# Kernel optimization log

Measured on AMD Instinct MI355X. Metric: run time of the kernel, lower is better.

## Reference

```python
import jax, jax.numpy as jnp
import numpy as np

N = 1_000_000
M = 8
HX = HY = 64
U = V = 512
L = 96 // 6  # latent_size // 6 = 16


def setup_inputs() -> dict:
    key = jax.random.key(0)
    ks = jax.random.split(key, 11)
    r = jax.random.uniform(ks[0], (N,), dtype=jnp.float32)
    m = jax.random.randint(ks[1], (N,), 0, M, dtype=jnp.int32)
    h = jax.random.uniform(ks[2], (N, 2), dtype=jnp.float32, minval=-1.0, maxval=1.0)
    u = jax.random.uniform(ks[3], (N,), dtype=jnp.float32)
    v = jax.random.uniform(ks[4], (N,), dtype=jnp.float32)
    Fxy = jax.random.normal(ks[5], (M, HX, HY, L), dtype=jnp.float32)
    Fxu = jax.random.normal(ks[6], (M, HX, U, L), dtype=jnp.float32)
    Fxv = jax.random.normal(ks[7], (M, HX, V, L), dtype=jnp.float32)
    Fyu = jax.random.normal(ks[8], (M, HY, U, L), dtype=jnp.float32)
    Fyv = jax.random.normal(ks[9], (M, HY, V, L), dtype=jnp.float32)
    Fuv = jax.random.normal(ks[10], (M, U, V, L), dtype=jnp.float32)
    return {"r": r, "m": m, "h": h, "u": u, "v": v,
            "Fxy": Fxy, "Fxu": Fxu, "Fxv": Fxv,
            "Fyu": Fyu, "Fyv": Fyv, "Fuv": Fuv}


def _bilinear(x, m, i, j, I, J):
    # x: [M, I, J, L]; m,i,j: [N]; wrap-around bilinear interpolation
    i1 = jnp.floor(i).astype(jnp.int32)
    j1 = jnp.floor(j).astype(jnp.int32)
    i2 = (i1 + 1) % I
    j2 = (j1 + 1) % J
    ir = (i - i1)[..., None]  # [N,1]
    jr = (j - j1)[..., None]
    top = x[m, i1, j1, :] * (1 - ir) + x[m, i2, j1, :] * ir
    bot = x[m, i1, j2, :] * (1 - ir) + x[m, i2, j2, :] * ir
    return top * (1 - jr) + bot * jr


def reference(r, m, h, u, v, Fxy, Fxu, Fxv, Fyu, Fyv, Fuv) -> jnp.ndarray:
    ind_hx = (h[..., 0] + 1) / 2 * HX
    ind_hy = (h[..., 1] + 1) / 2 * HY
    ind_hx = jnp.where(ind_hx == HX, HX - 1, ind_hx)
    ind_hy = jnp.where(ind_hy == HY, HY - 1, ind_hy)
    ind_u = u * U
    ind_v = v * V
    ind_u = jnp.where(ind_u == U, U - 1, ind_u)
    ind_v = jnp.where(ind_v == V, V - 1, ind_v)
    latent = jnp.concatenate([
        _bilinear(Fxy, m, ind_hx, ind_hy, HX, HY),
        _bilinear(Fxu, m, ind_hx, ind_u, HX, U),
        _bilinear(Fxv, m, ind_hx, ind_v, HX, V),
        _bilinear(Fyu, m, ind_hy, ind_u, HY, U),
        _bilinear(Fyv, m, ind_hy, ind_v, HY, V),
        _bilinear(Fuv, m, ind_u, ind_v, U, V),
    ], axis=-1)  # [N, 6*L]
    return latent
```

## Files before the change

kernel.cpp:

```cpp
#include <hip/hip_runtime.h>

#define HXc 64
#define HYc 64
#define Uc  512
#define Vc  512
#define Lc  16
#define NBUCK 8192

typedef float v4f __attribute__((ext_vector_type(4)));


__device__ __forceinline__ void compute_inds(float h0, float h1, float uu, float vv,
                                             float& ix, float& iy, float& iu, float& iv) {
    ix = (h0 + 1.0f) * 0.5f * (float)HXc; if (ix == (float)HXc) ix = (float)(HXc - 1);
    iy = (h1 + 1.0f) * 0.5f * (float)HYc; if (iy == (float)HYc) iy = (float)(HYc - 1);
    iu = uu * (float)Uc;                  if (iu == (float)Uc)  iu = (float)(Uc - 1);
    iv = vv * (float)Vc;                  if (iv == (float)Vc)  iv = (float)(Vc - 1);
}

__device__ __forceinline__ int bucket_of(int mm, float iu, float iv) {
    int us = ((int)iu) >> 4;
    int vs = ((int)iv) >> 4;
    return (((mm << 5) | vs) << 5) | us;
}


__global__ __launch_bounds__(256) void zero_kernel(int* __restrict__ counts) {
    int i = blockIdx.x * 256 + threadIdx.x;
    if (i < NBUCK) counts[i] = 0;
}


__global__ __launch_bounds__(256) void hist_kernel(
    const int* __restrict__ m_arr, const float* __restrict__ u_arr,
    const float* __restrict__ v_arr, int* __restrict__ counts, int N)
{
    int n = blockIdx.x * 256 + threadIdx.x;
    if (n >= N) return;
    float iu = u_arr[n] * (float)Uc; if (iu == (float)Uc) iu = (float)(Uc - 1);
    float iv = v_arr[n] * (float)Vc; if (iv == (float)Vc) iv = (float)(Vc - 1);
    atomicAdd(&counts[bucket_of(m_arr[n], iu, iv)], 1);
}


__global__ __launch_bounds__(1024) void scan_kernel(
    const int* __restrict__ counts, int* __restrict__ cursors)
{
    __shared__ int lds[1024];
    int t = threadIdx.x;
    int base = t * 8;
    int s = 0;
    #pragma unroll
    for (int k = 0; k < 8; ++k) s += counts[base + k];
    lds[t] = s;
    __syncthreads();
    for (int off = 1; off < 1024; off <<= 1) {
        int val = (t >= off) ? lds[t - off] : 0;
        __syncthreads();
        lds[t] += val;
        __syncthreads();
    }
    int run = lds[t] - s;
    #pragma unroll
    for (int k = 0; k < 8; ++k) {
        cursors[base + k] = run;
        run += counts[base + k];
    }
}


__global__ __launch_bounds__(256) void scatter_kernel(
    const int* __restrict__ m_arr, const float* __restrict__ h,
    const float* __restrict__ u_arr, const float* __restrict__ v_arr,
    int* __restrict__ cursors,
    v4f* __restrict__ inds4, int* __restrict__ m_s, int* __restrict__ outidx,
    int N)
{
    int n = blockIdx.x * 256 + threadIdx.x;
    if (n >= N) return;
    float h0 = h[2 * n], h1 = h[2 * n + 1];
    float ix, iy, iu, iv;
    compute_inds(h0, h1, u_arr[n], v_arr[n], ix, iy, iu, iv);
    int mm = m_arr[n];
    int b  = bucket_of(mm, iu, iv);
    int pos = atomicAdd(&cursors[b], 1);
    v4f rec; rec.x = ix; rec.y = iy; rec.z = iu; rec.w = iv;
    inds4[pos]  = rec;
    m_s[pos]    = mm;
    outidx[pos] = n;
}


struct BL {
    const float* a11; const float* a21; const float* a12; const float* a22;
    float ir, jr;
};

__device__ __forceinline__ v4f ld4(const float* p) {
    return *reinterpret_cast<const v4f*>(p);
}

__device__ __forceinline__ BL mk(const float* __restrict__ base, int mm,
                                 float fi, float fj, int I, int J, int chan) {
    BL b;
    int i1 = (int)floorf(fi);
    int j1 = (int)floorf(fj);
    b.ir = fi - (float)i1;
    b.jr = fj - (float)j1;
    int i2 = (i1 + 1 == I) ? 0 : (i1 + 1);
    int j2 = (j1 + 1 == J) ? 0 : (j1 + 1);
    const float* p = base + ((size_t)mm * I * J) * Lc + chan;
    b.a11 = p + (size_t)(i1 * J + j1) * Lc;
    b.a21 = p + (size_t)(i2 * J + j1) * Lc;
    b.a12 = p + (size_t)(i1 * J + j2) * Lc;
    b.a22 = p + (size_t)(i2 * J + j2) * Lc;
    return b;
}

__device__ __forceinline__ v4f blend(v4f c11, v4f c21, v4f c12, v4f c22,
                                     float ir, float jr) {
    float oir = 1.0f - ir;
    float ojr = 1.0f - jr;
    v4f top = c11 * oir + c21 * ir;
    v4f bot = c12 * oir + c22 * ir;
    return top * ojr + bot * jr;
}

__global__ __launch_bounds__(256) void main_kernel(
    const v4f* __restrict__ inds4, const int* __restrict__ m_s,
    const int* __restrict__ outidx,
    const float* __restrict__ Fxy, const float* __restrict__ Fxu,
    const float* __restrict__ Fxv, const float* __restrict__ Fyu,
    const float* __restrict__ Fyv, const float* __restrict__ Fuv,
    float* __restrict__ out, int N, int nwg)
{
    int bid = blockIdx.x;
    int q = nwg >> 3, r = nwg & 7;
    int xcd = bid & 7, idx = bid >> 3;
    int swz = (xcd < r) ? (xcd * (q + 1) + idx) : (r * (q + 1) + (xcd - r) * q + idx);

    int t   = swz * 256 + threadIdx.x;
    int k   = t >> 2;
    int sub = t & 3;
    if (k >= N) return;

    v4f inds = inds4[k];
    int mm   = m_s[k];
    int n    = outidx[k];
    float ind_hx = inds.x, ind_hy = inds.y, ind_u = inds.z, ind_v = inds.w;

    int chan = sub * 4;

    BL b0 = mk(Fxy, mm, ind_hx, ind_hy, HXc, HYc, chan);
    BL b1 = mk(Fxu, mm, ind_hx, ind_u,  HXc, Uc,  chan);
    BL b2 = mk(Fxv, mm, ind_hx, ind_v,  HXc, Vc,  chan);
    BL b3 = mk(Fyu, mm, ind_hy, ind_u,  HYc, Uc,  chan);
    BL b4 = mk(Fyv, mm, ind_hy, ind_v,  HYc, Vc,  chan);
    BL b5 = mk(Fuv, mm, ind_u,  ind_v,  Uc,  Vc,  chan);

    v4f c0a = ld4(b0.a11); v4f c0b = ld4(b0.a21); v4f c0c = ld4(b0.a12); v4f c0d = ld4(b0.a22);
    v4f c1a = ld4(b1.a11); v4f c1b = ld4(b1.a21); v4f c1c = ld4(b1.a12); v4f c1d = ld4(b1.a22);
    v4f c2a = ld4(b2.a11); v4f c2b = ld4(b2.a21); v4f c2c = ld4(b2.a12); v4f c2d = ld4(b2.a22);
    v4f c3a = ld4(b3.a11); v4f c3b = ld4(b3.a21); v4f c3c = ld4(b3.a12); v4f c3d = ld4(b3.a22);
    v4f c4a = ld4(b4.a11); v4f c4b = ld4(b4.a21); v4f c4c = ld4(b4.a12); v4f c4d = ld4(b4.a22);
    v4f c5a = ld4(b5.a11); v4f c5b = ld4(b5.a21); v4f c5c = ld4(b5.a12); v4f c5d = ld4(b5.a22);

    __builtin_amdgcn_sched_barrier(0);

    float* o = out + (size_t)n * 96 + chan;

    *reinterpret_cast<v4f*>(o + 0 * Lc) = blend(c0a, c0b, c0c, c0d, b0.ir, b0.jr);
    *reinterpret_cast<v4f*>(o + 1 * Lc) = blend(c1a, c1b, c1c, c1d, b1.ir, b1.jr);
    *reinterpret_cast<v4f*>(o + 2 * Lc) = blend(c2a, c2b, c2c, c2d, b2.ir, b2.jr);
    *reinterpret_cast<v4f*>(o + 3 * Lc) = blend(c3a, c3b, c3c, c3d, b3.ir, b3.jr);
    *reinterpret_cast<v4f*>(o + 4 * Lc) = blend(c4a, c4b, c4c, c4d, b4.ir, b4.jr);
    *reinterpret_cast<v4f*>(o + 5 * Lc) = blend(c5a, c5b, c5c, c5d, b5.ir, b5.jr);
}


__global__ __launch_bounds__(256) void flat_kernel(
    const int*   __restrict__ m_arr,
    const float* __restrict__ h,
    const float* __restrict__ u_arr,
    const float* __restrict__ v_arr,
    const float* __restrict__ Fxy, const float* __restrict__ Fxu,
    const float* __restrict__ Fxv, const float* __restrict__ Fyu,
    const float* __restrict__ Fyv, const float* __restrict__ Fuv,
    float* __restrict__ out, int N)
{
    int tid = blockIdx.x * blockDim.x + threadIdx.x;
    int n   = tid >> 2;
    int sub = tid & 3;
    if (n >= N) return;

    float h0 = h[2 * n], h1 = h[2 * n + 1];
    float ind_hx, ind_hy, ind_u, ind_v;
    compute_inds(h0, h1, u_arr[n], v_arr[n], ind_hx, ind_hy, ind_u, ind_v);
    int mm = m_arr[n];
    int chan = sub * 4;

    BL b0 = mk(Fxy, mm, ind_hx, ind_hy, HXc, HYc, chan);
    BL b1 = mk(Fxu, mm, ind_hx, ind_u,  HXc, Uc,  chan);
    BL b2 = mk(Fxv, mm, ind_hx, ind_v,  HXc, Vc,  chan);
    BL b3 = mk(Fyu, mm, ind_hy, ind_u,  HYc, Uc,  chan);
    BL b4 = mk(Fyv, mm, ind_hy, ind_v,  HYc, Vc,  chan);
    BL b5 = mk(Fuv, mm, ind_u,  ind_v,  Uc,  Vc,  chan);

    v4f c0a = ld4(b0.a11); v4f c0b = ld4(b0.a21); v4f c0c = ld4(b0.a12); v4f c0d = ld4(b0.a22);
    v4f c1a = ld4(b1.a11); v4f c1b = ld4(b1.a21); v4f c1c = ld4(b1.a12); v4f c1d = ld4(b1.a22);
    v4f c2a = ld4(b2.a11); v4f c2b = ld4(b2.a21); v4f c2c = ld4(b2.a12); v4f c2d = ld4(b2.a22);
    v4f c3a = ld4(b3.a11); v4f c3b = ld4(b3.a21); v4f c3c = ld4(b3.a12); v4f c3d = ld4(b3.a22);
    v4f c4a = ld4(b4.a11); v4f c4b = ld4(b4.a21); v4f c4c = ld4(b4.a12); v4f c4d = ld4(b4.a22);
    v4f c5a = ld4(b5.a11); v4f c5b = ld4(b5.a21); v4f c5c = ld4(b5.a12); v4f c5d = ld4(b5.a22);

    __builtin_amdgcn_sched_barrier(0);

    float* o = out + (size_t)n * 96 + chan;
    *reinterpret_cast<v4f*>(o + 0 * Lc) = blend(c0a, c0b, c0c, c0d, b0.ir, b0.jr);
    *reinterpret_cast<v4f*>(o + 1 * Lc) = blend(c1a, c1b, c1c, c1d, b1.ir, b1.jr);
    *reinterpret_cast<v4f*>(o + 2 * Lc) = blend(c2a, c2b, c2c, c2d, b2.ir, b2.jr);
    *reinterpret_cast<v4f*>(o + 3 * Lc) = blend(c3a, c3b, c3c, c3d, b3.ir, b3.jr);
    *reinterpret_cast<v4f*>(o + 4 * Lc) = blend(c4a, c4b, c4c, c4d, b4.ir, b4.jr);
    *reinterpret_cast<v4f*>(o + 5 * Lc) = blend(c5a, c5b, c5c, c5d, b5.ir, b5.jr);
}


extern "C" void kernel_launch(void* const* d_in, const int* in_sizes, int n_in,
                              void* d_out, int out_size, void* d_ws, size_t ws_size,
                              hipStream_t stream) {
    const int*   m_arr = (const int*)  d_in[1];
    const float* h     = (const float*)d_in[2];
    const float* u_arr = (const float*)d_in[3];
    const float* v_arr = (const float*)d_in[4];
    const float* Fxy   = (const float*)d_in[5];
    const float* Fxu   = (const float*)d_in[6];
    const float* Fxv   = (const float*)d_in[7];
    const float* Fyu   = (const float*)d_in[8];
    const float* Fyv   = (const float*)d_in[9];
    const float* Fuv   = (const float*)d_in[10];
    float* out = (float*)d_out;

    int N = in_sizes[0];

    size_t off_counts  = 0;
    size_t off_cursors = off_counts  + (size_t)NBUCK * 4;
    size_t off_inds4   = off_cursors + (size_t)NBUCK * 4;
    size_t off_ms      = off_inds4   + (size_t)N * 16;
    size_t off_outidx  = off_ms      + (size_t)N * 4;
    size_t needed      = off_outidx  + (size_t)N * 4;

    if (d_ws == nullptr || ws_size < needed) {
        int total_threads = 4 * N;
        dim3 block(256);
        dim3 grid((total_threads + 255) / 256);
        flat_kernel<<<grid, block, 0, stream>>>(m_arr, h, u_arr, v_arr,
                                                Fxy, Fxu, Fxv, Fyu, Fyv, Fuv, out, N);
        return;
    }

    char* ws = (char*)d_ws;
    int* counts  = (int*)(ws + off_counts);
    int* cursors = (int*)(ws + off_cursors);
    v4f* inds4   = (v4f*)(ws + off_inds4);
    int* m_s     = (int*)(ws + off_ms);
    int* outidx  = (int*)(ws + off_outidx);

    dim3 blk(256);
    dim3 grdN((N + 255) / 256);

    zero_kernel<<<dim3((NBUCK + 255) / 256), blk, 0, stream>>>(counts);
    hist_kernel<<<grdN, blk, 0, stream>>>(m_arr, u_arr, v_arr, counts, N);
    scan_kernel<<<dim3(1), dim3(1024), 0, stream>>>(counts, cursors);
    scatter_kernel<<<grdN, blk, 0, stream>>>(m_arr, h, u_arr, v_arr, cursors,
                                             inds4, m_s, outidx, N);

    int total_threads = 4 * N;
    int nwg = (total_threads + 255) / 256;
    main_kernel<<<dim3(nwg), blk, 0, stream>>>(inds4, m_s, outidx,
                                               Fxy, Fxu, Fxv, Fyu, Fyv, Fuv,
                                               out, N, nwg);
}
```

Baseline: 787.2 us.

## Convert feature grids to fp16 each call and gather half-precision texels

Each call now converts all six fp32 feature grids to fp16 in the workspace. The main gather kernel then reads 8-element half vectors, with two threads per point instead of four, and blends in fp32. The scatter packs the material id and output index into one 32-bit key, and the histogram kernel handles four points per thread with vector loads. The aim is to halve gather bandwidth and per-point index traffic, at the cost of converting roughly 150 MB of grids (about 38M floats) on every call and of fp16 rounding error.

Result: no change. 779.9 us (-0.9%).

```diff
diff --git a/kernel.cpp b/kernel.cpp
--- a/kernel.cpp
+++ b/kernel.cpp
@@ -7,7 +7,8 @@
 #define Lc  16
 #define NBUCK 8192
 
-typedef float v4f __attribute__((ext_vector_type(4)));
+typedef float    v4f __attribute__((ext_vector_type(4)));
+typedef _Float16 h8  __attribute__((ext_vector_type(8)));
 
 
 __device__ __forceinline__ void compute_inds(float h0, float h1, float uu, float vv,
@@ -25,6 +26,21 @@
 }
 
 
+__global__ __launch_bounds__(256) void convert_kernel(
+    const float* __restrict__ src, _Float16* __restrict__ dst, int n8)
+{
+    int i = blockIdx.x * 256 + threadIdx.x;
+    if (i >= n8) return;
+    const v4f* s4 = reinterpret_cast<const v4f*>(src);
+    v4f a = s4[2 * i];
+    v4f b = s4[2 * i + 1];
+    h8 o;
+    o[0] = (_Float16)a.x; o[1] = (_Float16)a.y; o[2] = (_Float16)a.z; o[3] = (_Float16)a.w;
+    o[4] = (_Float16)b.x; o[5] = (_Float16)b.y; o[6] = (_Float16)b.z; o[7] = (_Float16)b.w;
+    *reinterpret_cast<h8*>(dst + 8 * (size_t)i) = o;
+}
+
+
 __global__ __launch_bounds__(256) void zero_kernel(int* __restrict__ counts) {
     int i = blockIdx.x * 256 + threadIdx.x;
     if (i < NBUCK) counts[i] = 0;
@@ -35,11 +51,25 @@
     const int* __restrict__ m_arr, const float* __restrict__ u_arr,
     const float* __restrict__ v_arr, int* __restrict__ counts, int N)
 {
-    int n = blockIdx.x * 256 + threadIdx.x;
-    if (n >= N) return;
-    float iu = u_arr[n] * (float)Uc; if (iu == (float)Uc) iu = (float)(Uc - 1);
-    float iv = v_arr[n] * (float)Vc; if (iv == (float)Vc) iv = (float)(Vc - 1);
-    atomicAdd(&counts[bucket_of(m_arr[n], iu, iv)], 1);
+    int base = (blockIdx.x * 256 + threadIdx.x) * 4;
+    if (base >= N) return;
+    if (base + 3 < N) {
+        v4f u4 = *reinterpret_cast<const v4f*>(u_arr + base);
+        v4f vv4 = *reinterpret_cast<const v4f*>(v_arr + base);
+        int4 m4 = *reinterpret_cast<const int4*>(m_arr + base);
+        #pragma unroll
+        for (int k = 0; k < 4; ++k) {
+            float iu = ((const float*)&u4)[k] * (float)Uc; if (iu == (float)Uc) iu = (float)(Uc - 1);
+            float iv = ((const float*)&vv4)[k] * (float)Vc; if (iv == (float)Vc) iv = (float)(Vc - 1);
+            atomicAdd(&counts[bucket_of(((const int*)&m4)[k], iu, iv)], 1);
+        }
+    } else {
+        for (int n = base; n < N; ++n) {
+            float iu = u_arr[n] * (float)Uc; if (iu == (float)Uc) iu = (float)(Uc - 1);
+            float iv = v_arr[n] * (float)Vc; if (iv == (float)Vc) iv = (float)(Vc - 1);
+            atomicAdd(&counts[bucket_of(m_arr[n], iu, iv)], 1);
+        }
+    }
 }
 
 
@@ -73,7 +103,7 @@
     const int* __restrict__ m_arr, const float* __restrict__ h,
     const float* __restrict__ u_arr, const float* __restrict__ v_arr,
     int* __restrict__ cursors,
-    v4f* __restrict__ inds4, int* __restrict__ m_s, int* __restrict__ outidx,
+    v4f* __restrict__ inds4, unsigned int* __restrict__ keys,
     int N)
 {
     int n = blockIdx.x * 256 + threadIdx.x;
@@ -85,9 +115,116 @@
     int b  = bucket_of(mm, iu, iv);
     int pos = atomicAdd(&cursors[b], 1);
     v4f rec; rec.x = ix; rec.y = iy; rec.z = iu; rec.w = iv;
-    inds4[pos]  = rec;
-    m_s[pos]    = mm;
-    outidx[pos] = n;
+    inds4[pos] = rec;
+    keys[pos]  = (unsigned int)n | ((unsigned int)mm << 24);
+}
+
+
+struct F8 { v4f lo, hi; };
+
+__device__ __forceinline__ F8 cvt8(h8 x) {
+    F8 r;
+    r.lo.x = (float)x[0]; r.lo.y = (float)x[1]; r.lo.z = (float)x[2]; r.lo.w = (float)x[3];
+    r.hi.x = (float)x[4]; r.hi.y = (float)x[5]; r.hi.z = (float)x[6]; r.hi.w = (float)x[7];
+    return r;
+}
+
+struct BLH {
+    const _Float16* a11; const _Float16* a21; const _Float16* a12; const _Float16* a22;
+    float ir, jr;
+};
+
+__device__ __forceinline__ BLH mkh(const _Float16* __restrict__ base, int mm,
+                                   float fi, float fj, int I, int J, int chan) {
+    BLH b;
+    int i1 = (int)floorf(fi);
+    int j1 = (int)floorf(fj);
+    b.ir = fi - (float)i1;
+    b.jr = fj - (float)j1;
+    int i2 = (i1 + 1 == I) ? 0 : (i1 + 1);
+    int j2 = (j1 + 1 == J) ? 0 : (j1 + 1);
+    const _Float16* p = base + ((size_t)mm * I * J) * Lc + chan;
+    b.a11 = p + (size_t)(i1 * J + j1) * Lc;
+    b.a21 = p + (size_t)(i2 * J + j1) * Lc;
+    b.a12 = p + (size_t)(i1 * J + j2) * Lc;
+    b.a22 = p + (size_t)(i2 * J + j2) * Lc;
+    return b;
+}
+
+__device__ __forceinline__ h8 ldh(const _Float16* p) {
+    return *reinterpret_cast<const h8*>(p);
+}
+
+__device__ __forceinline__ F8 blend8(h8 h11, h8 h21, h8 h12, h8 h22, float ir, float jr) {
+    F8 c11 = cvt8(h11), c21 = cvt8(h21), c12 = cvt8(h12), c22 = cvt8(h22);
+    float oir = 1.0f - ir, ojr = 1.0f - jr;
+    F8 r;
+    r.lo = (c11.lo * oir + c21.lo * ir) * ojr + (c12.lo * oir + c22.lo * ir) * jr;
+    r.hi = (c11.hi * oir + c21.hi * ir) * ojr + (c12.hi * oir + c22.hi * ir) * jr;
+    return r;
+}
+
+__global__ __launch_bounds__(256) void main_f16_kernel(
+    const v4f* __restrict__ inds4, const unsigned int* __restrict__ keys,
+    const _Float16* __restrict__ Hxy, const _Float16* __restrict__ Hxu,
+    const _Float16* __restrict__ Hxv, const _Float16* __restrict__ Hyu,
+    const _Float16* __restrict__ Hyv, const _Float16* __restrict__ Huv,
+    float* __restrict__ out, int N, int nwg)
+{
+    int bid = blockIdx.x;
+    int q = nwg >> 3, r = nwg & 7;
+    int xcd = bid & 7, idx = bid >> 3;
+    int swz = (xcd < r) ? (xcd * (q + 1) + idx) : (r * (q + 1) + (xcd - r) * q + idx);
+
+    int t   = swz * 256 + threadIdx.x;
+    int k   = t >> 1;
+    int sub = t & 1;
+    if (k >= N) return;
+
+    v4f inds = inds4[k];
+    unsigned int key = keys[k];
+    int mm = (int)(key >> 24);
+    int n  = (int)(key & 0xFFFFFFu);
+    float ind_hx = inds.x, ind_hy = inds.y, ind_u = inds.z, ind_v = inds.w;
+
+    int chan = sub * 8;
+
+    BLH b0 = mkh(Hxy, mm, ind_hx, ind_hy, HXc, HYc, chan);
+    BLH b1 = mkh(Hxu, mm, ind_hx, ind_u,  HXc, Uc,  chan);
+    BLH b2 = mkh(Hxv, mm, ind_hx, ind_v,  HXc, Vc,  chan);
+    BLH b3 = mkh(Hyu, mm, ind_hy, ind_u,  HYc, Uc,  chan);
+    BLH b4 = mkh(Hyv, mm, ind_hy, ind_v,  HYc, Vc,  chan);
+    BLH b5 = mkh(Huv, mm, ind_u,  ind_v,  Uc,  Vc,  chan);
+
+    h8 c0a = ldh(b0.a11); h8 c0b = ldh(b0.a21); h8 c0c = ldh(b0.a12); h8 c0d = ldh(b0.a22);
+    h8 c1a = ldh(b1.a11); h8 c1b = ldh(b1.a21); h8 c1c = ldh(b1.a12); h8 c1d = ldh(b1.a22);
+    h8 c2a = ldh(b2.a11); h8 c2b = ldh(b2.a21); h8 c2c = ldh(b2.a12); h8 c2d = ldh(b2.a22);
+    h8 c3a = ldh(b3.a11); h8 c3b = ldh(b3.a21); h8 c3c = ldh(b3.a12); h8 c3d = ldh(b3.a22);
+    h8 c4a = ldh(b4.a11); h8 c4b = ldh(b4.a21); h8 c4c = ldh(b4.a12); h8 c4d = ldh(b4.a22);
+    h8 c5a = ldh(b5.a11); h8 c5b = ldh(b5.a21); h8 c5c = ldh(b5.a12); h8 c5d = ldh(b5.a22);
+
+    __builtin_amdgcn_sched_barrier(0);
+
+    float* o = out + (size_t)n * 96 + chan;
+
+    F8 r0 = blend8(c0a, c0b, c0c, c0d, b0.ir, b0.jr);
+    *reinterpret_cast<v4f*>(o + 0 * Lc)     = r0.lo;
+    *reinterpret_cast<v4f*>(o + 0 * Lc + 4) = r0.hi;
+    F8 r1 = blend8(c1a, c1b, c1c, c1d, b1.ir, b1.jr);
+    *reinterpret_cast<v4f*>(o + 1 * Lc)     = r1.lo;
+    *reinterpret_cast<v4f*>(o + 1 * Lc + 4) = r1.hi;
+    F8 r2 = blend8(c2a, c2b, c2c, c2d, b2.ir, b2.jr);
+    *reinterpret_cast<v4f*>(o + 2 * Lc)     = r2.lo;
+    *reinterpret_cast<v4f*>(o + 2 * Lc + 4) = r2.hi;
+    F8 r3 = blend8(c3a, c3b, c3c, c3d, b3.ir, b3.jr);
+    *reinterpret_cast<v4f*>(o + 3 * Lc)     = r3.lo;
+    *reinterpret_cast<v4f*>(o + 3 * Lc + 4) = r3.hi;
+    F8 r4 = blend8(c4a, c4b, c4c, c4d, b4.ir, b4.jr);
+    *reinterpret_cast<v4f*>(o + 4 * Lc)     = r4.lo;
+    *reinterpret_cast<v4f*>(o + 4 * Lc + 4) = r4.hi;
+    F8 r5 = blend8(c5a, c5b, c5c, c5d, b5.ir, b5.jr);
+    *reinterpret_cast<v4f*>(o + 5 * Lc)     = r5.lo;
+    *reinterpret_cast<v4f*>(o + 5 * Lc + 4) = r5.hi;
 }
 
 
@@ -126,9 +263,8 @@
     return top * ojr + bot * jr;
 }
 
-__global__ __launch_bounds__(256) void main_kernel(
-    const v4f* __restrict__ inds4, const int* __restrict__ m_s,
-    const int* __restrict__ outidx,
+__global__ __launch_bounds__(256) void main_f32_kernel(
+    const v4f* __restrict__ inds4, const unsigned int* __restrict__ keys,
     const float* __restrict__ Fxy, const float* __restrict__ Fxu,
     const float* __restrict__ Fxv, const float* __restrict__ Fyu,
     const float* __restrict__ Fyv, const float* __restrict__ Fuv,
@@ -145,8 +281,9 @@
     if (k >= N) return;
 
     v4f inds = inds4[k];
-    int mm   = m_s[k];
-    int n    = outidx[k];
+    unsigned int key = keys[k];
+    int mm = (int)(key >> 24);
+    int n  = (int)(key & 0xFFFFFFu);
     float ind_hx = inds.x, ind_hy = inds.y, ind_u = inds.z, ind_v = inds.w;
 
     int chan = sub * 4;
@@ -168,7 +305,6 @@
     __builtin_amdgcn_sched_barrier(0);
 
     float* o = out + (size_t)n * 96 + chan;
-
     *reinterpret_cast<v4f*>(o + 0 * Lc) = blend(c0a, c0b, c0c, c0d, b0.ir, b0.jr);
     *reinterpret_cast<v4f*>(o + 1 * Lc) = blend(c1a, c1b, c1c, c1d, b1.ir, b1.jr);
     *reinterpret_cast<v4f*>(o + 2 * Lc) = blend(c2a, c2b, c2c, c2d, b2.ir, b2.jr);
@@ -242,41 +378,87 @@
 
     int N = in_sizes[0];
 
-    size_t off_counts  = 0;
+    const size_t SZ_xy = (size_t)8 * 64 * 64 * 16;
+    const size_t SZ_mid = (size_t)8 * 64 * 512 * 16;
+    const size_t SZ_uv = (size_t)8 * 512 * 512 * 16;
+    const size_t SZ_half_total = SZ_xy + 4 * SZ_mid + SZ_uv;
+
+    size_t off_hxy   = 0;
+    size_t off_hxu   = off_hxy + SZ_xy * 2;
+    size_t off_hxv   = off_hxu + SZ_mid * 2;
+    size_t off_hyu   = off_hxv + SZ_mid * 2;
+    size_t off_hyv   = off_hyu + SZ_mid * 2;
+    size_t off_huv   = off_hyv + SZ_mid * 2;
+    size_t off_counts  = off_huv + SZ_uv * 2;
     size_t off_cursors = off_counts  + (size_t)NBUCK * 4;
     size_t off_inds4   = off_cursors + (size_t)NBUCK * 4;
-    size_t off_ms      = off_inds4   + (size_t)N * 16;
-    size_t off_outidx  = off_ms      + (size_t)N * 4;
-    size_t needed      = off_outidx  + (size_t)N * 4;
-
-    if (d_ws == nullptr || ws_size < needed) {
-        int total_threads = 4 * N;
-        dim3 block(256);
-        dim3 grid((total_threads + 255) / 256);
-        flat_kernel<<<grid, block, 0, stream>>>(m_arr, h, u_arr, v_arr,
-                                                Fxy, Fxu, Fxv, Fyu, Fyv, Fuv, out, N);
-        return;
-    }
-
-    char* ws = (char*)d_ws;
-    int* counts  = (int*)(ws + off_counts);
-    int* cursors = (int*)(ws + off_cursors);
-    v4f* inds4   = (v4f*)(ws + off_inds4);
-    int* m_s     = (int*)(ws + off_ms);
-    int* outidx  = (int*)(ws + off_outidx);
+    size_t off_keys    = off_inds4   + (size_t)N * 16;
+    size_t need_f16    = off_keys    + (size_t)N * 4;
+
+    size_t f32_counts  = 0;
+    size_t f32_cursors = f32_counts  + (size_t)NBUCK * 4;
+    size_t f32_inds4   = f32_cursors + (size_t)NBUCK * 4;
+    size_t f32_keys    = f32_inds4   + (size_t)N * 16;
+    size_t need_f32    = f32_keys    + (size_t)N * 4;
 
     dim3 blk(256);
     dim3 grdN((N + 255) / 256);
-
-    zero_kernel<<<dim3((NBUCK + 255) / 256), blk, 0, stream>>>(counts);
-    hist_kernel<<<grdN, blk, 0, stream>>>(m_arr, u_arr, v_arr, counts, N);
-    scan_kernel<<<dim3(1), dim3(1024), 0, stream>>>(counts, cursors);
-    scatter_kernel<<<grdN, blk, 0, stream>>>(m_arr, h, u_arr, v_arr, cursors,
-                                             inds4, m_s, outidx, N);
-
-    int total_threads = 4 * N;
-    int nwg = (total_threads + 255) / 256;
-    main_kernel<<<dim3(nwg), blk, 0, stream>>>(inds4, m_s, outidx,
-                                               Fxy, Fxu, Fxv, Fyu, Fyv, Fuv,
-                                               out, N, nwg);
-}
+    char* ws = (char*)d_ws;
+
+    if (ws != nullptr && ws_size >= need_f16) {
+        _Float16* Hxy = (_Float16*)(ws + off_hxy);
+        _Float16* Hxu = (_Float16*)(ws + off_hxu);
+        _Float16* Hxv = (_Float16*)(ws + off_hxv);
+        _Float16* Hyu = (_Float16*)(ws + off_hyu);
+        _Float16* Hyv = (_Float16*)(ws + off_hyv);
+        _Float16* Huv = (_Float16*)(ws + off_huv);
+        int* counts  = (int*)(ws + off_counts);
+        int* cursors = (int*)(ws + off_cursors);
+        v4f* inds4   = (v4f*)(ws + off_inds4);
+        unsigned int* keys = (unsigned int*)(ws + off_keys);
+
+        int n8_xy  = (int)(SZ_xy  / 8);
+        int n8_mid = (int)(SZ_mid / 8);
+        int n8_uv  = (int)(SZ_uv  / 8);
+        convert_kernel<<<dim3((n8_xy  + 255) / 256), blk, 0, stream>>>(Fxy, Hxy, n8_xy);
+        convert_kernel<<<dim3((n8_mid + 255) / 256), blk, 0, stream>>>(Fxu, Hxu, n8_mid);
+        convert_kernel<<<dim3((n8_mid + 255) / 256), blk, 0, stream>>>(Fxv, Hxv, n8_mid);
+        convert_kernel<<<dim3((n8_mid + 255) / 256), blk, 0, stream>>>(Fyu, Hyu, n8_mid);
+        convert_kernel<<<dim3((n8_mid + 255) / 256), blk, 0, stream>>>(Fyv, Hyv, n8_mid);
+        convert_kernel<<<dim3((n8_uv  + 255) / 256), blk, 0, stream>>>(Fuv, Huv, n8_uv);
+
+        zero_kernel<<<dim3((NBUCK + 255) / 256), blk, 0, stream>>>(counts);
+        hist_kernel<<<dim3((N / 4 + 255) / 256), blk, 0, stream>>>(m_arr, u_arr, v_arr, counts, N);
+        scan_kernel<<<dim3(1), dim3(1024), 0, stream>>>(counts, cursors);
+        scatter_kernel<<<grdN, blk, 0, stream>>>(m_arr, h, u_arr, v_arr, cursors,
+                                                 inds4, keys, N);
+
+        int total_threads = 2 * N;
+        int nwg = (total_threads + 255) / 256;
+        main_f16_kernel<<<dim3(nwg), blk, 0, stream>>>(inds4, keys,
+                                                       Hxy, Hxu, Hxv, Hyu, Hyv, Huv,
+                                                       out, N, nwg);
+    } else if (ws != nullptr && ws_size >= need_f32) {
+        int* counts  = (int*)(ws + f32_counts);
+        int* cursors = (int*)(ws + f32_cursors);
+        v4f* inds4   = (v4f*)(ws + f32_inds4);
+        unsigned int* keys = (unsigned int*)(ws + f32_keys);
+
+        zero_kernel<<<dim3((NBUCK + 255) / 256), blk, 0, stream>>>(counts);
+        hist_kernel<<<dim3((N / 4 + 255) / 256), blk, 0, stream>>>(m_arr, u_arr, v_arr, counts, N);
+        scan_kernel<<<dim3(1), dim3(1024), 0, stream>>>(counts, cursors);
+        scatter_kernel<<<grdN, blk, 0, stream>>>(m_arr, h, u_arr, v_arr, cursors,
+                                                 inds4, keys, N);
+
+        int total_threads = 4 * N;
+        int nwg = (total_threads + 255) / 256;
+        main_f32_kernel<<<dim3(nwg), blk, 0, stream>>>(inds4, keys,
+                                                       Fxy, Fxu, Fxv, Fyu, Fyv, Fuv,
+                                                       out, N, nwg);
+    } else {
+        int total_threads = 4 * N;
+        dim3 grid((total_threads + 255) / 256);
+        flat_kernel<<<grid, blk, 0, stream>>>(m_arr, h, u_arr, v_arr,
+                                              Fxy, Fxu, Fxv, Fyu, Fyv, Fuv, out, N);
+    }
+}
```
